# Kernel optimization log

Hardware: AMD Instinct MI355X
Metric: run time of the kernel (lower is better)

Reference implementation:

```python
import jax, jax.numpy as jnp
import numpy as np

B, T_AUX, UP = 4, 75, 110
N_AUX, N_Q, HID, SKIP = 54, 256, 192, 256
K, AUX_K = 6, 3
DIL_FACTS = [0, 1, 2] * 3  # dilation_depth=3, dilation_repeat=3
T = T_AUX * UP - 1  # 8249


def conv1d(x, w, b, dil=1, pad=(0, 0)):
    # x: (B,C,T), w: (O,I,K) torch Conv1d layout
    if pad != (0, 0):
        x = jnp.pad(x, ((0, 0), (0, 0), pad))
    y = jax.lax.conv_general_dilated(x, w, (1,), 'VALID', rhs_dilation=(dil,),
                                     dimension_numbers=('NCH', 'OIH', 'NCH'))
    return y + b[None, :, None]


def setup_inputs() -> dict:
    key = jax.random.key(0)
    ks = jax.random.split(key, 24)
    s = 0.05
    inp = {
        'audio': jax.random.normal(ks[0], (B, N_Q, T), jnp.float32),
        'aux': jax.random.normal(ks[1], (B, N_AUX, T_AUX), jnp.float32),
        'scale_in_w': jax.random.normal(ks[2], (N_AUX, N_AUX, 1), jnp.float32) * s,
        'scale_in_b': jax.random.normal(ks[3], (N_AUX,), jnp.float32) * s,
        'aux0_w': jax.random.normal(ks[4], (N_AUX * 3, N_AUX, AUX_K), jnp.float32) * s,
        'aux0_b': jax.random.normal(ks[5], (N_AUX * 3,), jnp.float32) * s,
        'aux1_w': jax.random.normal(ks[6], (N_AUX * 9, N_AUX * 3, AUX_K), jnp.float32) * s,
        'aux1_b': jax.random.normal(ks[7], (N_AUX * 9,), jnp.float32) * s,
        'up_w': jax.random.normal(ks[8], (UP,), jnp.float32) * s,
        'up_b': jax.random.normal(ks[9], (), jnp.float32) * s,
        'causal_w': jax.random.normal(ks[10], (HID, N_Q, K), jnp.float32) * s,
        'causal_b': jax.random.normal(ks[11], (HID,), jnp.float32) * s,
        'inx_w': jax.random.normal(ks[12], (9, 2 * HID, N_AUX * 9, 1), jnp.float32) * s,
        'inx_b': jax.random.normal(ks[13], (9, 2 * HID), jnp.float32) * s,
        'dilh_w': jax.random.normal(ks[14], (9, 2 * HID, HID, K), jnp.float32) * s,
        'dilh_b': jax.random.normal(ks[15], (9, 2 * HID), jnp.float32) * s,
        'skip_w': jax.random.normal(ks[16], (9, SKIP, HID, 1), jnp.float32) * s,
        'skip_b': jax.random.normal(ks[17], (9, SKIP), jnp.float32) * s,
        'out1_w': jax.random.normal(ks[18], (N_Q, SKIP, 1), jnp.float32) * s,
        'out1_b': jax.random.normal(ks[19], (N_Q,), jnp.float32) * s,
        'out2_w': jax.random.normal(ks[20], (N_Q, N_Q, 1), jnp.float32) * s,
        'out2_b': jax.random.normal(ks[21], (N_Q,), jnp.float32) * s,
    }
    return inp


def reference(audio, aux, scale_in_w, scale_in_b, aux0_w, aux0_b, aux1_w, aux1_b,
              up_w, up_b, causal_w, causal_b, inx_w, inx_b, dilh_w, dilh_b,
              skip_w, skip_b, out1_w, out1_b, out2_w, out2_b):
    # conditioning path: scale_in -> two-sided dilated convs -> deconv upsample
    a = conv1d(aux, scale_in_w, scale_in_b)
    a = conv1d(a, aux0_w, aux0_b, dil=1, pad=(1, 1))      # k=3, dil=1, same length
    a = conv1d(a, aux1_w, aux1_b, dil=3, pad=(3, 3))      # k=3, dil=3, same length
    b_, c_, t_ = a.shape
    x = (a[:, :, :, None] * up_w).reshape(b_, c_, t_ * UP) + up_b  # ConvTranspose2d(1,1,(1,UP))
    x = x[:, :, 1:]  # (B, 486, T)
    # audio path: causal conv (left pad k-1) + softsign
    h = jax.nn.soft_sign(conv1d(audio, causal_w, causal_b, dil=1, pad=(K - 1, 0)))
    sum_out = None
    for l, d in enumerate(DIL_FACTS):
        dil = K ** d
        lpad = dil * (K - 1)  # k**(d+1) - k**d
        xh = conv1d(x, inx_w[l], inx_b[l]) * conv1d(h, dilh_w[l], dilh_b[l], dil=dil, pad=(lpad, 0))
        z = jax.nn.sigmoid(xh[:, :HID])
        h = (1.0 - z) * jnp.tanh(xh[:, HID:]) + z * h
        skip = conv1d(h, skip_w[l], skip_b[l])
        sum_out = skip if sum_out is None else sum_out + skip
    out = conv1d(jax.nn.relu(sum_out), out1_w, out1_b)
    out = conv1d(jax.nn.relu(out), out2_w, out2_b)
    return out.transpose(0, 2, 1)  # (B, T, n_quantize)
```

## Files before the change

kernel.cpp:

```cpp
#include <hip/hip_runtime.h>

#define TLEN 8249
#define TPAD 8320
#define NTILES 130
#define NB 4
#define NAUX 54
#define NQ 256
#define HID 192
#define NSKIP 256
#define KW 6
#define UPF 110
#define TAUX 75
#define PADR 180
#define HROWS (PADR + TPAD)

typedef __attribute__((ext_vector_type(8))) short bf16x8v;
typedef __attribute__((ext_vector_type(4))) float f32x4;

__device__ __forceinline__ unsigned short f2bf(float f) {
  unsigned int u = __float_as_uint(f);
  u += 0x7FFFu + ((u >> 16) & 1u);
  return (unsigned short)(u >> 16);
}

__device__ __forceinline__ f32x4 mfma16(bf16x8v a, bf16x8v b, f32x4 c) {
  return __builtin_amdgcn_mfma_f32_16x16x32_bf16(a, b, c, 0, 0, 0);
}

__global__ void prepack_kernel(
    const float* causal_w, const float* dilh_w, const float* skip_w,
    const float* out1_w, const float* out2_w,
    const float* inx_w, const float* inx_b, const float* up_b,
    unsigned short* pk_causal, unsigned short* pk_dilh, unsigned short* pk_skip,
    unsigned short* pk_out1, unsigned short* pk_out2, float* Cbuf)
{
  int i = blockIdx.x * blockDim.x + threadIdx.x;
  if (i < 9*6*6*24*64*8) {
    int t = i;
    int j = t & 7; t >>= 3;
    int lane = t & 63; t >>= 6;
    int nf = t % 24; t /= 24;
    int kc = t % 6; t /= 6;
    int tap = t % 6; t /= 6;
    int l = t;
    int oc = nf*16 + (lane & 15);
    int ic = kc*32 + ((lane >> 4) << 3) + j;
    pk_dilh[i] = f2bf(dilh_w[((l*384 + oc)*HID + ic)*KW + tap]);
  }
  if (i < 6*8*12*64*8) {
    int t = i;
    int j = t & 7; t >>= 3;
    int lane = t & 63; t >>= 6;
    int nf = t % 12; t /= 12;
    int kc = t % 8; t /= 8;
    int tap = t;
    int oc = nf*16 + (lane & 15);
    int ic = kc*32 + ((lane >> 4) << 3) + j;
    pk_causal[i] = f2bf(causal_w[(oc*NQ + ic)*KW + tap]);
  }
  if (i < 9*6*16*64*8) {
    int t = i;
    int j = t & 7; t >>= 3;
    int lane = t & 63; t >>= 6;
    int nf = t % 16; t /= 16;
    int kc = t % 6; t /= 6;
    int l = t;
    int sc = nf*16 + (lane & 15);
    int ic = kc*32 + ((lane >> 4) << 3) + j;
    pk_skip[i] = f2bf(skip_w[(l*NSKIP + sc)*HID + ic]);
  }
  if (i < 8*16*64*8) {
    int t = i;
    int j = t & 7; t >>= 3;
    int lane = t & 63; t >>= 6;
    int nf = t % 16; t /= 16;
    int kc = t;
    int oq = nf*16 + (lane & 15);
    int sc = kc*32 + ((lane >> 4) << 3) + j;
    pk_out1[i] = f2bf(out1_w[oq*NSKIP + sc]);
    pk_out2[i] = f2bf(out2_w[oq*NQ + sc]);
  }
  if (i < 9*384) {
    int l = i / 384, oc = i % 384;
    const float* wr = inx_w + (l*384 + oc)*486;
    float s = 0.f;
    for (int c = 0; c < 486; c++) s += wr[c];
    Cbuf[i] = up_b[0]*s + inx_b[i];
  }
}

__global__ void zpad_kernel(unsigned short* h_all) {
  int i = blockIdx.x*blockDim.x + threadIdx.x;
  if (i < 9*NB*PADR*HID) {
    int slab = i / (NB*PADR*HID), r = i % (NB*PADR*HID);
    int b = r / (PADR*HID), rr = r % (PADR*HID);
    h_all[((size_t)slab*NB + b)*HROWS*HID + rr] = 0;
  }
}

__global__ void aux1_kernel(const float* aux, const float* w, const float* bias, float* a1) {
  int q = blockIdx.x, b = blockIdx.y, co = threadIdx.x;
  if (co >= NAUX) return;
  float acc = bias[co];
  for (int ci = 0; ci < NAUX; ci++)
    acc += w[co*NAUX + ci] * aux[(b*NAUX + ci)*TAUX + q];
  a1[(b*NAUX + co)*TAUX + q] = acc;
}

__global__ void aux2_kernel(const float* a1, const float* w, const float* bias, float* a2) {
  __shared__ float s[3][NAUX];
  int q = blockIdx.x, b = blockIdx.y, tid = threadIdx.x;
  for (int i = tid; i < 3*NAUX; i += blockDim.x) {
    int k = i / NAUX, c = i % NAUX;
    int qq = q - 1 + k;
    s[k][c] = (qq >= 0 && qq < TAUX) ? a1[(b*NAUX + c)*TAUX + qq] : 0.f;
  }
  __syncthreads();
  int co = tid;
  if (co >= 162) return;
  float acc = bias[co];
  for (int c = 0; c < NAUX; c++)
    #pragma unroll
    for (int k = 0; k < 3; k++)
      acc += w[(co*NAUX + c)*3 + k] * s[k][c];
  a2[(b*162 + co)*TAUX + q] = acc;
}

__global__ void aux3_kernel(const float* a2, const float* w, const float* bias, float* a3) {
  __shared__ float s[3][162];
  int q = blockIdx.x, b = blockIdx.y, tid = threadIdx.x;
  for (int i = tid; i < 3*162; i += blockDim.x) {
    int k = i / 162, c = i % 162;
    int qq = q + 3*(k - 1);
    s[k][c] = (qq >= 0 && qq < TAUX) ? a2[(b*162 + c)*TAUX + qq] : 0.f;
  }
  __syncthreads();
  int co = tid;
  if (co >= 486) return;
  float acc = bias[co];
  for (int c = 0; c < 162; c++)
    #pragma unroll
    for (int k = 0; k < 3; k++)
      acc += w[(co*162 + c)*3 + k] * s[k][c];
  a3[(b*486 + co)*TAUX + q] = acc;
}

__global__ void g_kernel(const float* a3, const float* inx_w, float* G) {
  __shared__ float s[486][15];
  int q0 = blockIdx.x * 15, b = blockIdx.y, l = blockIdx.z;
  int tid = threadIdx.x;
  for (int i = tid; i < 486*15; i += 384) {
    int c = i / 15, qq = i % 15;
    s[c][qq] = a3[(b*486 + c)*TAUX + q0 + qq];
  }
  __syncthreads();
  int oc = tid;
  float acc[15];
  #pragma unroll
  for (int qq = 0; qq < 15; qq++) acc[qq] = 0.f;
  const float* wrow = inx_w + (l*384 + oc)*486;
  for (int c = 0; c < 486; c++) {
    float w = wrow[c];
    #pragma unroll
    for (int qq = 0; qq < 15; qq++) acc[qq] += w * s[c][qq];
  }
  for (int qq = 0; qq < 15; qq++)
    G[((size_t)(l*NB + b)*TAUX + q0 + qq)*384 + oc] = acc[qq];
}

__global__ __launch_bounds__(256, 2)
void causal_kernel(const float* audio, const unsigned short* pk, const float* cb,
                   unsigned short* hbf)
{
  __shared__ __align__(16) unsigned short sA[72*264];
  int b = blockIdx.y, t0 = blockIdx.x*64, tid = threadIdx.x;
  int wv = tid >> 6, lane = tid & 63, lanelo = lane & 15;

  for (int i = tid; i < 72*256; i += 256) {
    int ic = i / 72, tt = i % 72;
    int t = t0 - 5 + tt;
    float v = (t >= 0 && t < TLEN) ? audio[(size_t)(b*NQ + ic)*TLEN + t] : 0.f;
    sA[tt*264 + ic] = f2bf(v);
  }
  __syncthreads();

  f32x4 acc[4][3];
  f32x4 z4 = {0.f, 0.f, 0.f, 0.f};
  #pragma unroll
  for (int m = 0; m < 4; m++)
    #pragma unroll
    for (int i = 0; i < 3; i++) acc[m][i] = z4;

  for (int tap = 0; tap < 6; tap++) {
    for (int kc = 0; kc < 8; kc++) {
      bf16x8v A[4];
      int ko = kc*32 + ((lane >> 4) << 3);
      #pragma unroll
      for (int m = 0; m < 4; m++)
        A[m] = *(const bf16x8v*)&sA[(m*16 + lanelo + tap)*264 + ko];
      #pragma unroll
      for (int i = 0; i < 3; i++) {
        int nf = wv*3 + i;
        bf16x8v Bf = *(const bf16x8v*)&pk[(size_t)((((tap*8) + kc)*12 + nf)*64 + lane)*8];
        #pragma unroll
        for (int m = 0; m < 4; m++) acc[m][i] = mfma16(A[m], Bf, acc[m][i]);
      }
    }
  }

  #pragma unroll
  for (int m = 0; m < 4; m++)
    #pragma unroll
    for (int i = 0; i < 3; i++) {
      int oc = (wv*3 + i)*16 + lanelo;
      float bias = cb[oc];
      #pragma unroll
      for (int r = 0; r < 4; r++) {
        int tl = m*16 + ((lane >> 4) << 2) + r;
        int t = t0 + tl;
        float v = acc[m][i][r] + bias;
        float h0 = v / (1.f + fabsf(v));
        hbf[(size_t)(b*HROWS + t + PADR)*HID + oc] = f2bf(h0);
      }
    }
}

__global__ __launch_bounds__(512, 4)
void layer_kernel(int dil,
                  const unsigned short* __restrict__ hin,
                  unsigned short* __restrict__ hout,
                  const unsigned short* __restrict__ pk_dilh_l,
                  const float* __restrict__ dilh_b_l,
                  const float* __restrict__ Gl, const float* __restrict__ Cl,
                  const float* __restrict__ up_w)
{
  __shared__ __align__(16) unsigned short hs[2][64*192];
  int b = blockIdx.y, t0 = blockIdx.x*64, tid = threadIdx.x;
  int wv = tid >> 6, lane = tid & 63, lanelo = lane & 15, lanehi = lane >> 4;
  int mwv = wv >> 2, nwv = wv & 3;

  const size_t hbase = (size_t)b * HROWS * HID;
  int rowbase0 = t0 - 5*dil + PADR;

  uint4 st[3];
  {
    #pragma unroll
    for (int j = 0; j < 3; j++) {
      int c = tid + j*512, row = c/24, cbk = c%24;
      st[j] = *(const uint4*)&hin[hbase + (size_t)(rowbase0+row)*HID + cbk*8];
    }
    #pragma unroll
    for (int j = 0; j < 3; j++) {
      int c = tid + j*512, row = c/24, cbk = c%24;
      *(uint4*)&hs[0][row*192 + ((cbk ^ (row&7))<<3)] = st[j];
    }
  }

  f32x4 accz[2][3], acct[2][3];
  f32x4 z4 = {0.f, 0.f, 0.f, 0.f};
  #pragma unroll
  for (int m = 0; m < 2; m++)
    #pragma unroll
    for (int i = 0; i < 3; i++) { accz[m][i] = z4; acct[m][i] = z4; }

  for (int tap = 0; tap < 6; tap++) {
    __syncthreads();
    if (tap < 5) {
      int rb = rowbase0 + (tap+1)*dil;
      #pragma unroll
      for (int j = 0; j < 3; j++) {
        int c = tid + j*512, row = c/24, cbk = c%24;
        st[j] = *(const uint4*)&hin[hbase + (size_t)(rb+row)*HID + cbk*8];
      }
    }
    const unsigned short* bufc = hs[tap & 1];
    #pragma unroll
    for (int kc = 0; kc < 6; kc++) {
      bf16x8v A[2];
      #pragma unroll
      for (int m = 0; m < 2; m++) {
        int r = mwv*32 + m*16 + lanelo;
        int cbk = kc*4 + lanehi;
        A[m] = *(const bf16x8v*)&bufc[r*192 + ((cbk ^ (r&7))<<3)];
      }
      #pragma unroll
      for (int i = 0; i < 3; i++) {
        const unsigned short* bp =
            &pk_dilh_l[(size_t)(((tap*6 + kc)*24 + nwv*3 + i)*64 + lane)*8];
        bf16x8v Bz = *(const bf16x8v*)bp;
        bf16x8v Bt = *(const bf16x8v*)(bp + 12*512);
        #pragma unroll
        for (int m = 0; m < 2; m++) {
          accz[m][i] = mfma16(A[m], Bz, accz[m][i]);
          acct[m][i] = mfma16(A[m], Bt, acct[m][i]);
        }
      }
    }
    if (tap < 5) {
      unsigned short* bufn = hs[(tap+1) & 1];
      #pragma unroll
      for (int j = 0; j < 3; j++) {
        int c = tid + j*512, row = c/24, cbk = c%24;
        *(uint4*)&bufn[row*192 + ((cbk ^ (row&7))<<3)] = st[j];
      }
    }
  }

  float izc[3], itc[3], bzc[3], btc[3];
  #pragma unroll
  for (int i = 0; i < 3; i++) {
    int ocz = (nwv*3 + i)*16 + lanelo;
    izc[i] = Cl[ocz];       itc[i] = Cl[192 + ocz];
    bzc[i] = dilh_b_l[ocz]; btc[i] = dilh_b_l[192 + ocz];
  }
  #pragma unroll
  for (int m = 0; m < 2; m++) {
    #pragma unroll
    for (int r = 0; r < 4; r++) {
      int tl = mwv*32 + m*16 + (lanehi << 2) + r;
      int t = t0 + tl;
      int tp1 = t + 1;
      int q = tp1 / UPF; if (q > TAUX - 1) q = TAUX - 1;
      int ui = tp1 - q*UPF; if (ui > UPF - 1) ui = UPF - 1;
      float u = up_w[ui];
      const float* Gb = Gl + (size_t)(b*TAUX + q)*384;
      #pragma unroll
      for (int i = 0; i < 3; i++) {
        int ocz = (nwv*3 + i)*16 + lanelo;
        float iz = u*Gb[ocz]       + izc[i];
        float it = u*Gb[192 + ocz] + itc[i];
        float xz = (accz[m][i][r] + bzc[i]) * iz;
        float xt = (acct[m][i][r] + btc[i]) * it;
        float z  = 1.f / (1.f + __expf(-xz));
        float e2 = __expf(2.f*xt);
        float th = 1.f - 2.f/(e2 + 1.f);
        int cbh = ocz >> 3, jh = ocz & 7;
        unsigned short hob = hs[1][tl*192 + ((cbh ^ (tl&7))<<3) + jh];
        float hold = __uint_as_float(((unsigned int)hob) << 16);
        float hn = (1.f - z)*th + z*hold;
        hout[hbase + (size_t)(t0 + tl + PADR)*HID + ocz] = f2bf(hn);
      }
    }
  }
}

__global__ __launch_bounds__(512, 2)
void skipsum_kernel(const unsigned short* __restrict__ h_all,
                    const unsigned short* __restrict__ pk_skip,
                    const float* __restrict__ skip_b,
                    unsigned short* __restrict__ sbuf)
{
  extern __shared__ __align__(16) unsigned short ss[];
  int b = blockIdx.y, t0 = blockIdx.x*128, tid = threadIdx.x;
  int wv = tid >> 6, lane = tid & 63, lanelo = lane & 15, lanehi = lane >> 4;
  int mwv = wv >> 2, nwv = wv & 3;
  const size_t HS = (size_t)NB * HROWS * HID;

  auto hsrc = [&](int l) {
    int slab = (l == 8) ? 0 : (l + 1);
    return h_all + (size_t)slab*HS + (size_t)b*HROWS*HID + (size_t)(t0 + PADR)*HID;
  };

  uint4 st[6];
  {
    const unsigned short* src = hsrc(0);
    #pragma unroll
    for (int j = 0; j < 6; j++) {
      int c = tid + j*512, row = c/24, cbk = c%24;
      st[j] = *(const uint4*)&src[(size_t)row*HID + cbk*8];
    }
    #pragma unroll
    for (int j = 0; j < 6; j++) {
      int c = tid + j*512, row = c/24, cbk = c%24;
      *(uint4*)&ss[row*192 + ((cbk ^ (row&7))<<3)] = st[j];
    }
  }

  f32x4 acc[4][4];
  f32x4 z4 = {0.f, 0.f, 0.f, 0.f};
  #pragma unroll
  for (int m = 0; m < 4; m++)
    #pragma unroll
    for (int i = 0; i < 4; i++) acc[m][i] = z4;

  for (int l = 0; l < 9; l++) {
    __syncthreads();
    if (l < 8) {
      const unsigned short* src = hsrc(l + 1);
      #pragma unroll
      for (int j = 0; j < 6; j++) {
        int c = tid + j*512, row = c/24, cbk = c%24;
        st[j] = *(const uint4*)&src[(size_t)row*HID + cbk*8];
      }
    }
    const unsigned short* bufc = ss + (l & 1)*(128*192);
    #pragma unroll
    for (int kc = 0; kc < 6; kc++) {
      bf16x8v A[4];
      #pragma unroll
      for (int m = 0; m < 4; m++) {
        int r = mwv*64 + m*16 + lanelo;
        int cbk = kc*4 + lanehi;
        A[m] = *(const bf16x8v*)&bufc[r*192 + ((cbk ^ (r&7))<<3)];
      }
      #pragma unroll
      for (int i = 0; i < 4; i++) {
        bf16x8v Bf = *(const bf16x8v*)
            &pk_skip[(size_t)(((l*6 + kc)*16 + nwv*4 + i)*64 + lane)*8];
        #pragma unroll
        for (int m = 0; m < 4; m++) acc[m][i] = mfma16(A[m], Bf, acc[m][i]);
      }
    }
    if (l < 8) {
      unsigned short* bufn = ss + ((l+1) & 1)*(128*192);
      #pragma unroll
      for (int j = 0; j < 6; j++) {
        int c = tid + j*512, row = c/24, cbk = c%24;
        *(uint4*)&bufn[row*192 + ((cbk ^ (row&7))<<3)] = st[j];
      }
    }
  }

  #pragma unroll
  for (int i = 0; i < 4; i++) {
    int sc = (nwv*4 + i)*16 + lanelo;
    float bias = 0.f;
    #pragma unroll
    for (int l = 0; l < 9; l++) bias += skip_b[l*NSKIP + sc];
    #pragma unroll
    for (int m = 0; m < 4; m++) {
      #pragma unroll
      for (int r = 0; r < 4; r++) {
        int tl = mwv*64 + m*16 + (lanehi << 2) + r;
        float v = acc[m][i][r] + bias;
        sbuf[(size_t)(b*TPAD + t0 + tl)*NSKIP + sc] = f2bf(fmaxf(v, 0.f));
      }
    }
  }
}

__global__ __launch_bounds__(256, 2)
void out_kernel(const unsigned short* sbuf, const unsigned short* pk1, const float* b1,
                const unsigned short* pk2, const float* b2, float* dout)
{
  __shared__ __align__(16) unsigned short s0[64*264];
  int b = blockIdx.y, t0 = blockIdx.x*64, tid = threadIdx.x;
  int wv = tid >> 6, lane = tid & 63, lanelo = lane & 15;
  f32x4 z4 = {0.f, 0.f, 0.f, 0.f};

  for (int i = tid; i < 64*32; i += 256) {
    int r = i >> 5, cbk = i & 31;
    *(uint4*)&s0[r*264 + cbk*8] =
        *(const uint4*)&sbuf[(size_t)(b*TPAD + t0 + r)*NSKIP + cbk*8];
  }
  __syncthreads();

  f32x4 acc[4][4];
  #pragma unroll
  for (int m = 0; m < 4; m++)
    #pragma unroll
    for (int i = 0; i < 4; i++) acc[m][i] = z4;
  for (int kc = 0; kc < 8; kc++) {
    bf16x8v A[4];
    int ko = kc*32 + ((lane >> 4) << 3);
    #pragma unroll
    for (int m = 0; m < 4; m++)
      A[m] = *(const bf16x8v*)&s0[(m*16 + lanelo)*264 + ko];
    #pragma unroll
    for (int i = 0; i < 4; i++) {
      int nf = wv*4 + i;
      bf16x8v Bf = *(const bf16x8v*)&pk1[(size_t)((kc*16 + nf)*64 + lane)*8];
      #pragma unroll
      for (int m = 0; m < 4; m++) acc[m][i] = mfma16(A[m], Bf, acc[m][i]);
    }
  }
  __syncthreads();
  #pragma unroll
  for (int m = 0; m < 4; m++)
    #pragma unroll
    for (int i = 0; i < 4; i++) {
      int oq = (wv*4 + i)*16 + lanelo;
      float bias = b1[oq];
      #pragma unroll
      for (int r = 0; r < 4; r++) {
        int tl = m*16 + ((lane >> 4) << 2) + r;
        float v = acc[m][i][r] + bias;
        s0[tl*264 + oq] = f2bf(fmaxf(v, 0.f));
      }
    }
  __syncthreads();

  #pragma unroll
  for (int m = 0; m < 4; m++)
    #pragma unroll
    for (int i = 0; i < 4; i++) acc[m][i] = z4;
  for (int kc = 0; kc < 8; kc++) {
    bf16x8v A[4];
    int ko = kc*32 + ((lane >> 4) << 3);
    #pragma unroll
    for (int m = 0; m < 4; m++)
      A[m] = *(const bf16x8v*)&s0[(m*16 + lanelo)*264 + ko];
    #pragma unroll
    for (int i = 0; i < 4; i++) {
      int nf = wv*4 + i;
      bf16x8v Bf = *(const bf16x8v*)&pk2[(size_t)((kc*16 + nf)*64 + lane)*8];
      #pragma unroll
      for (int m = 0; m < 4; m++) acc[m][i] = mfma16(A[m], Bf, acc[m][i]);
    }
  }
  #pragma unroll
  for (int m = 0; m < 4; m++)
    #pragma unroll
    for (int i = 0; i < 4; i++) {
      int oq = (wv*4 + i)*16 + lanelo;
      float bias = b2[oq];
      #pragma unroll
      for (int r = 0; r < 4; r++) {
        int tl = m*16 + ((lane >> 4) << 2) + r;
        int t = t0 + tl;
        if (t < TLEN) dout[(size_t)(b*TLEN + t)*NQ + oq] = acc[m][i][r] + bias;
      }
    }
}

extern "C" void kernel_launch(void* const* d_in, const int* in_sizes, int n_in,
                              void* d_out, int out_size, void* d_ws, size_t ws_size,
                              hipStream_t stream)
{
  const float* audio      = (const float*)d_in[0];
  const float* aux        = (const float*)d_in[1];
  const float* scale_in_w = (const float*)d_in[2];
  const float* scale_in_b = (const float*)d_in[3];
  const float* aux0_w     = (const float*)d_in[4];
  const float* aux0_b     = (const float*)d_in[5];
  const float* aux1_w     = (const float*)d_in[6];
  const float* aux1_b     = (const float*)d_in[7];
  const float* up_w       = (const float*)d_in[8];
  const float* up_b       = (const float*)d_in[9];
  const float* causal_w   = (const float*)d_in[10];
  const float* causal_b   = (const float*)d_in[11];
  const float* inx_w      = (const float*)d_in[12];
  const float* inx_b      = (const float*)d_in[13];
  const float* dilh_w     = (const float*)d_in[14];
  const float* dilh_b     = (const float*)d_in[15];
  const float* skip_w     = (const float*)d_in[16];
  const float* skip_b     = (const float*)d_in[17];
  const float* out1_w     = (const float*)d_in[18];
  const float* out1_b     = (const float*)d_in[19];
  const float* out2_w     = (const float*)d_in[20];
  const float* out2_b     = (const float*)d_in[21];

  char* ws = (char*)d_ws;
  size_t off = 0;
  auto alloc = [&](size_t bytes) -> void* {
    void* p = ws + off;
    off += (bytes + 255) & ~(size_t)255;
    return p;
  };
  unsigned short* pk_causal = (unsigned short*)alloc((size_t)6*8*12*64*8*2);
  unsigned short* pk_dilh   = (unsigned short*)alloc((size_t)9*6*6*24*64*8*2);
  unsigned short* pk_skip   = (unsigned short*)alloc((size_t)9*6*16*64*8*2);
  unsigned short* pk_out1   = (unsigned short*)alloc((size_t)8*16*64*8*2);
  unsigned short* pk_out2   = (unsigned short*)alloc((size_t)8*16*64*8*2);
  float* Cbuf    = (float*)alloc((size_t)9*384*4);
  float* a1      = (float*)alloc((size_t)NB*NAUX*TAUX*4);
  float* a2      = (float*)alloc((size_t)NB*162*TAUX*4);
  float* a3      = (float*)alloc((size_t)NB*486*TAUX*4);
  float* Gbuf    = (float*)alloc((size_t)9*NB*TAUX*384*4);
  const size_t HS = (size_t)NB*HROWS*HID;
  unsigned short* h_all = (unsigned short*)alloc((size_t)9*HS*2);
  unsigned short* sbuf  = (unsigned short*)alloc((size_t)NB*TPAD*NSKIP*2);

  hipFuncSetAttribute((const void*)skipsum_kernel,
                      hipFuncAttributeMaxDynamicSharedMemorySize, 2*128*192*2);

  hipLaunchKernelGGL(prepack_kernel, dim3((9*6*6*24*64*8 + 255)/256), dim3(256), 0, stream,
                     causal_w, dilh_w, skip_w, out1_w, out2_w, inx_w, inx_b, up_b,
                     pk_causal, pk_dilh, pk_skip, pk_out1, pk_out2, Cbuf);
  hipLaunchKernelGGL(zpad_kernel, dim3((9*NB*PADR*HID + 255)/256), dim3(256), 0, stream,
                     h_all);
  hipLaunchKernelGGL(aux1_kernel, dim3(TAUX, NB), dim3(64), 0, stream,
                     aux, scale_in_w, scale_in_b, a1);
  hipLaunchKernelGGL(aux2_kernel, dim3(TAUX, NB), dim3(192), 0, stream,
                     a1, aux0_w, aux0_b, a2);
  hipLaunchKernelGGL(aux3_kernel, dim3(TAUX, NB), dim3(512), 0, stream,
                     a2, aux1_w, aux1_b, a3);
  hipLaunchKernelGGL(g_kernel, dim3(5, NB, 9), dim3(384), 0, stream,
                     a3, inx_w, Gbuf);
  hipLaunchKernelGGL(causal_kernel, dim3(NTILES, NB), dim3(256), 0, stream,
                     audio, pk_causal, causal_b, h_all );

  const int dils[9] = {1, 6, 36, 1, 6, 36, 1, 6, 36};
  for (int l = 0; l < 9; l++) {
    const unsigned short* hin = h_all + (size_t)l*HS;
    unsigned short* hout      = (l == 8) ? h_all : h_all + (size_t)(l+1)*HS;
    hipLaunchKernelGGL(layer_kernel, dim3(NTILES, NB), dim3(512), 0, stream,
                       dils[l], hin, hout,
                       pk_dilh + (size_t)l*6*6*24*64*8,
                       dilh_b + (size_t)l*384,
                       Gbuf + (size_t)l*NB*TAUX*384,
                       Cbuf + (size_t)l*384,
                       up_w);
  }

  hipLaunchKernelGGL(skipsum_kernel, dim3(TPAD/128, NB), dim3(512), 2*128*192*2, stream,
                     h_all, pk_skip, skip_b, sbuf);
  hipLaunchKernelGGL(out_kernel, dim3(NTILES, NB), dim3(256), 0, stream,
                     sbuf, pk_out1, out1_b, pk_out2, out2_b, (float*)d_out);
}
```

Before: 1.067 ms.

## Load dilated-conv halo window once into LDS and shrink skipsum tiles

For dilations 1 and 6, the layer kernel loads a single halo window of 64+5*dil rows into shared memory once and reads all six taps from it at shifted row offsets. This replaces six per-tap global reloads that mostly overlapped, and it also supplies the old-h values for the gate from the same buffer. Dilation 36 keeps the double-buffered per-tap path. Separately, skipsum now uses 64-row tiles with static shared memory and targets 4 blocks per CU instead of 2, which gives more blocks and occupancy but less B-fragment reuse per block.

```diff
diff --git a/kernel.cpp b/kernel.cpp
--- a/kernel.cpp
+++ b/kernel.cpp
@@ -242,8 +242,53 @@
   const size_t hbase = (size_t)b * HROWS * HID;
   int rowbase0 = t0 - 5*dil + PADR;
 
-  uint4 st[3];
-  {
+  f32x4 accz[2][3], acct[2][3];
+  f32x4 z4 = {0.f, 0.f, 0.f, 0.f};
+  #pragma unroll
+  for (int m = 0; m < 2; m++)
+    #pragma unroll
+    for (int i = 0; i < 3; i++) { accz[m][i] = z4; acct[m][i] = z4; }
+
+  const unsigned short* holdbuf;
+  int holdoff;
+  unsigned short* flat = &hs[0][0];
+
+  if (dil != 36) {
+    int W = 64 + 5*dil;
+    for (int c = tid; c < W*24; c += 512) {
+      int row = c/24, cbk = c%24;
+      uint4 v = *(const uint4*)&hin[hbase + (size_t)(rowbase0+row)*HID + cbk*8];
+      *(uint4*)&flat[row*192 + ((cbk ^ (row&7))<<3)] = v;
+    }
+    __syncthreads();
+    for (int tap = 0; tap < 6; tap++) {
+      int rb = mwv*32 + lanelo + tap*dil;
+      #pragma unroll
+      for (int kc = 0; kc < 6; kc++) {
+        bf16x8v A[2];
+        #pragma unroll
+        for (int m = 0; m < 2; m++) {
+          int r = rb + m*16;
+          int cbk = kc*4 + lanehi;
+          A[m] = *(const bf16x8v*)&flat[r*192 + ((cbk ^ (r&7))<<3)];
+        }
+        #pragma unroll
+        for (int i = 0; i < 3; i++) {
+          const unsigned short* bp =
+              &pk_dilh_l[(size_t)(((tap*6 + kc)*24 + nwv*3 + i)*64 + lane)*8];
+          bf16x8v Bz = *(const bf16x8v*)bp;
+          bf16x8v Bt = *(const bf16x8v*)(bp + 12*512);
+          #pragma unroll
+          for (int m = 0; m < 2; m++) {
+            accz[m][i] = mfma16(A[m], Bz, accz[m][i]);
+            acct[m][i] = mfma16(A[m], Bt, acct[m][i]);
+          }
+        }
+      }
+    }
+    holdbuf = flat; holdoff = 5*dil;
+  } else {
+    uint4 st[3];
     #pragma unroll
     for (int j = 0; j < 3; j++) {
       int c = tid + j*512, row = c/24, cbk = c%24;
@@ -254,56 +299,49 @@
       int c = tid + j*512, row = c/24, cbk = c%24;
       *(uint4*)&hs[0][row*192 + ((cbk ^ (row&7))<<3)] = st[j];
     }
-  }
-
-  f32x4 accz[2][3], acct[2][3];
-  f32x4 z4 = {0.f, 0.f, 0.f, 0.f};
-  #pragma unroll
-  for (int m = 0; m < 2; m++)
-    #pragma unroll
-    for (int i = 0; i < 3; i++) { accz[m][i] = z4; acct[m][i] = z4; }
-
-  for (int tap = 0; tap < 6; tap++) {
-    __syncthreads();
-    if (tap < 5) {
-      int rb = rowbase0 + (tap+1)*dil;
-      #pragma unroll
-      for (int j = 0; j < 3; j++) {
-        int c = tid + j*512, row = c/24, cbk = c%24;
-        st[j] = *(const uint4*)&hin[hbase + (size_t)(rb+row)*HID + cbk*8];
-      }
-    }
-    const unsigned short* bufc = hs[tap & 1];
-    #pragma unroll
-    for (int kc = 0; kc < 6; kc++) {
-      bf16x8v A[2];
-      #pragma unroll
-      for (int m = 0; m < 2; m++) {
-        int r = mwv*32 + m*16 + lanelo;
-        int cbk = kc*4 + lanehi;
-        A[m] = *(const bf16x8v*)&bufc[r*192 + ((cbk ^ (r&7))<<3)];
-      }
-      #pragma unroll
-      for (int i = 0; i < 3; i++) {
-        const unsigned short* bp =
-            &pk_dilh_l[(size_t)(((tap*6 + kc)*24 + nwv*3 + i)*64 + lane)*8];
-        bf16x8v Bz = *(const bf16x8v*)bp;
-        bf16x8v Bt = *(const bf16x8v*)(bp + 12*512);
+    for (int tap = 0; tap < 6; tap++) {
+      __syncthreads();
+      if (tap < 5) {
+        int rb = rowbase0 + (tap+1)*36;
+        #pragma unroll
+        for (int j = 0; j < 3; j++) {
+          int c = tid + j*512, row = c/24, cbk = c%24;
+          st[j] = *(const uint4*)&hin[hbase + (size_t)(rb+row)*HID + cbk*8];
+        }
+      }
+      const unsigned short* bufc = hs[tap & 1];
+      #pragma unroll
+      for (int kc = 0; kc < 6; kc++) {
+        bf16x8v A[2];
         #pragma unroll
         for (int m = 0; m < 2; m++) {
-          accz[m][i] = mfma16(A[m], Bz, accz[m][i]);
-          acct[m][i] = mfma16(A[m], Bt, acct[m][i]);
+          int r = mwv*32 + m*16 + lanelo;
+          int cbk = kc*4 + lanehi;
+          A[m] = *(const bf16x8v*)&bufc[r*192 + ((cbk ^ (r&7))<<3)];
         }
-      }
-    }
-    if (tap < 5) {
-      unsigned short* bufn = hs[(tap+1) & 1];
-      #pragma unroll
-      for (int j = 0; j < 3; j++) {
-        int c = tid + j*512, row = c/24, cbk = c%24;
-        *(uint4*)&bufn[row*192 + ((cbk ^ (row&7))<<3)] = st[j];
-      }
-    }
+        #pragma unroll
+        for (int i = 0; i < 3; i++) {
+          const unsigned short* bp =
+              &pk_dilh_l[(size_t)(((tap*6 + kc)*24 + nwv*3 + i)*64 + lane)*8];
+          bf16x8v Bz = *(const bf16x8v*)bp;
+          bf16x8v Bt = *(const bf16x8v*)(bp + 12*512);
+          #pragma unroll
+          for (int m = 0; m < 2; m++) {
+            accz[m][i] = mfma16(A[m], Bz, accz[m][i]);
+            acct[m][i] = mfma16(A[m], Bt, acct[m][i]);
+          }
+        }
+      }
+      if (tap < 5) {
+        unsigned short* bufn = hs[(tap+1) & 1];
+        #pragma unroll
+        for (int j = 0; j < 3; j++) {
+          int c = tid + j*512, row = c/24, cbk = c%24;
+          *(uint4*)&bufn[row*192 + ((cbk ^ (row&7))<<3)] = st[j];
+        }
+      }
+    }
+    holdbuf = &hs[1][0]; holdoff = 0;
   }
 
   float izc[3], itc[3], bzc[3], btc[3];
@@ -319,6 +357,7 @@
     for (int r = 0; r < 4; r++) {
       int tl = mwv*32 + m*16 + (lanehi << 2) + r;
       int t = t0 + tl;
+      int hr = tl + holdoff;
       int tp1 = t + 1;
       int q = tp1 / UPF; if (q > TAUX - 1) q = TAUX - 1;
       int ui = tp1 - q*UPF; if (ui > UPF - 1) ui = UPF - 1;
@@ -335,23 +374,23 @@
         float e2 = __expf(2.f*xt);
         float th = 1.f - 2.f/(e2 + 1.f);
         int cbh = ocz >> 3, jh = ocz & 7;
-        unsigned short hob = hs[1][tl*192 + ((cbh ^ (tl&7))<<3) + jh];
+        unsigned short hob = holdbuf[hr*192 + ((cbh ^ (hr&7))<<3) + jh];
         float hold = __uint_as_float(((unsigned int)hob) << 16);
         float hn = (1.f - z)*th + z*hold;
-        hout[hbase + (size_t)(t0 + tl + PADR)*HID + ocz] = f2bf(hn);
-      }
-    }
-  }
-}
-
-__global__ __launch_bounds__(512, 2)
+        hout[hbase + (size_t)(t + PADR)*HID + ocz] = f2bf(hn);
+      }
+    }
+  }
+}
+
+__global__ __launch_bounds__(512, 4)
 void skipsum_kernel(const unsigned short* __restrict__ h_all,
                     const unsigned short* __restrict__ pk_skip,
                     const float* __restrict__ skip_b,
                     unsigned short* __restrict__ sbuf)
 {
-  extern __shared__ __align__(16) unsigned short ss[];
-  int b = blockIdx.y, t0 = blockIdx.x*128, tid = threadIdx.x;
+  __shared__ __align__(16) unsigned short ss[2][64*192];
+  int b = blockIdx.y, t0 = blockIdx.x*64, tid = threadIdx.x;
   int wv = tid >> 6, lane = tid & 63, lanelo = lane & 15, lanehi = lane >> 4;
   int mwv = wv >> 2, nwv = wv & 3;
   const size_t HS = (size_t)NB * HROWS * HID;
@@ -361,25 +400,25 @@
     return h_all + (size_t)slab*HS + (size_t)b*HROWS*HID + (size_t)(t0 + PADR)*HID;
   };
 
-  uint4 st[6];
+  uint4 st[3];
   {
     const unsigned short* src = hsrc(0);
     #pragma unroll
-    for (int j = 0; j < 6; j++) {
+    for (int j = 0; j < 3; j++) {
       int c = tid + j*512, row = c/24, cbk = c%24;
       st[j] = *(const uint4*)&src[(size_t)row*HID + cbk*8];
     }
     #pragma unroll
-    for (int j = 0; j < 6; j++) {
+    for (int j = 0; j < 3; j++) {
       int c = tid + j*512, row = c/24, cbk = c%24;
-      *(uint4*)&ss[row*192 + ((cbk ^ (row&7))<<3)] = st[j];
-    }
-  }
-
-  f32x4 acc[4][4];
+      *(uint4*)&ss[0][row*192 + ((cbk ^ (row&7))<<3)] = st[j];
+    }
+  }
+
+  f32x4 acc[2][4];
   f32x4 z4 = {0.f, 0.f, 0.f, 0.f};
   #pragma unroll
-  for (int m = 0; m < 4; m++)
+  for (int m = 0; m < 2; m++)
     #pragma unroll
     for (int i = 0; i < 4; i++) acc[m][i] = z4;
 
@@ -388,18 +427,18 @@
     if (l < 8) {
       const unsigned short* src = hsrc(l + 1);
       #pragma unroll
-      for (int j = 0; j < 6; j++) {
+      for (int j = 0; j < 3; j++) {
         int c = tid + j*512, row = c/24, cbk = c%24;
         st[j] = *(const uint4*)&src[(size_t)row*HID + cbk*8];
       }
     }
-    const unsigned short* bufc = ss + (l & 1)*(128*192);
+    const unsigned short* bufc = ss[l & 1];
     #pragma unroll
     for (int kc = 0; kc < 6; kc++) {
-      bf16x8v A[4];
-      #pragma unroll
-      for (int m = 0; m < 4; m++) {
-        int r = mwv*64 + m*16 + lanelo;
+      bf16x8v A[2];
+      #pragma unroll
+      for (int m = 0; m < 2; m++) {
+        int r = mwv*32 + m*16 + lanelo;
         int cbk = kc*4 + lanehi;
         A[m] = *(const bf16x8v*)&bufc[r*192 + ((cbk ^ (r&7))<<3)];
       }
@@ -408,13 +447,13 @@
         bf16x8v Bf = *(const bf16x8v*)
             &pk_skip[(size_t)(((l*6 + kc)*16 + nwv*4 + i)*64 + lane)*8];
         #pragma unroll
-        for (int m = 0; m < 4; m++) acc[m][i] = mfma16(A[m], Bf, acc[m][i]);
+        for (int m = 0; m < 2; m++) acc[m][i] = mfma16(A[m], Bf, acc[m][i]);
       }
     }
     if (l < 8) {
-      unsigned short* bufn = ss + ((l+1) & 1)*(128*192);
-      #pragma unroll
-      for (int j = 0; j < 6; j++) {
+      unsigned short* bufn = ss[(l+1) & 1];
+      #pragma unroll
+      for (int j = 0; j < 3; j++) {
         int c = tid + j*512, row = c/24, cbk = c%24;
         *(uint4*)&bufn[row*192 + ((cbk ^ (row&7))<<3)] = st[j];
       }
@@ -428,10 +467,10 @@
     #pragma unroll
     for (int l = 0; l < 9; l++) bias += skip_b[l*NSKIP + sc];
     #pragma unroll
-    for (int m = 0; m < 4; m++) {
+    for (int m = 0; m < 2; m++) {
       #pragma unroll
       for (int r = 0; r < 4; r++) {
-        int tl = mwv*64 + m*16 + (lanehi << 2) + r;
+        int tl = mwv*32 + m*16 + (lanehi << 2) + r;
         float v = acc[m][i][r] + bias;
         sbuf[(size_t)(b*TPAD + t0 + tl)*NSKIP + sc] = f2bf(fmaxf(v, 0.f));
       }
@@ -571,9 +610,6 @@
   unsigned short* h_all = (unsigned short*)alloc((size_t)9*HS*2);
   unsigned short* sbuf  = (unsigned short*)alloc((size_t)NB*TPAD*NSKIP*2);
 
-  hipFuncSetAttribute((const void*)skipsum_kernel,
-                      hipFuncAttributeMaxDynamicSharedMemorySize, 2*128*192*2);
-
   hipLaunchKernelGGL(prepack_kernel, dim3((9*6*6*24*64*8 + 255)/256), dim3(256), 0, stream,
                      causal_w, dilh_w, skip_w, out1_w, out2_w, inx_w, inx_b, up_b,
                      pk_causal, pk_dilh, pk_skip, pk_out1, pk_out2, Cbuf);
@@ -603,7 +639,7 @@
                        up_w);
   }
 
-  hipLaunchKernelGGL(skipsum_kernel, dim3(TPAD/128, NB), dim3(512), 2*128*192*2, stream,
+  hipLaunchKernelGGL(skipsum_kernel, dim3(NTILES, NB), dim3(512), 0, stream,
                      h_all, pk_skip, skip_b, sbuf);
   hipLaunchKernelGGL(out_kernel, dim3(NTILES, NB), dim3(256), 0, stream,
                      sbuf, pk_out1, out1_b, pk_out2, out2_b, (float*)d_out);
```

Measured after the change: 958.5 us. -10.1%, faster.

## Load full dilated halo once per layer tile, fuse skip and output kernels

Applied to the files above, without the earlier changes.

The layer kernel now handles 128 time steps per block. It loads the whole dilated window (128+5*dil rows) into dynamic LDS once, replacing the per-tap double-buffered reloads, so overlapping tap rows are shared. Outputs are staged through LDS for coalesced 16-byte stores in both the causal and layer kernels. The skip-sum and the two output convolutions are fused into one tail kernel, which removes the sbuf round-trip through global memory and writes the final output coalesced via LDS. The cost is much larger LDS use per block (up to about 120KB for dil=36) and half as many blocks, which lowers occupancy and parallelism.

```diff
diff --git a/kernel.cpp b/kernel.cpp
--- a/kernel.cpp
+++ b/kernel.cpp
@@ -3,6 +3,7 @@
 #define TLEN 8249
 #define TPAD 8320
 #define NTILES 130
+#define NTILES2 65
 #define NB 4
 #define NAUX 54
 #define NQ 256
@@ -174,7 +175,7 @@
 {
   __shared__ __align__(16) unsigned short sA[72*264];
   int b = blockIdx.y, t0 = blockIdx.x*64, tid = threadIdx.x;
-  int wv = tid >> 6, lane = tid & 63, lanelo = lane & 15;
+  int wv = tid >> 6, lane = tid & 63, lanelo = lane & 15, lanehi = lane >> 4;
 
   for (int i = tid; i < 72*256; i += 256) {
     int ic = i / 72, tt = i % 72;
@@ -194,7 +195,7 @@
   for (int tap = 0; tap < 6; tap++) {
     for (int kc = 0; kc < 8; kc++) {
       bf16x8v A[4];
-      int ko = kc*32 + ((lane >> 4) << 3);
+      int ko = kc*32 + (lanehi << 3);
       #pragma unroll
       for (int m = 0; m < 4; m++)
         A[m] = *(const bf16x8v*)&sA[(m*16 + lanelo + tap)*264 + ko];
@@ -208,6 +209,7 @@
     }
   }
 
+  unsigned short hv[4][3][4];
   #pragma unroll
   for (int m = 0; m < 4; m++)
     #pragma unroll
@@ -216,16 +218,33 @@
       float bias = cb[oc];
       #pragma unroll
       for (int r = 0; r < 4; r++) {
-        int tl = m*16 + ((lane >> 4) << 2) + r;
-        int t = t0 + tl;
         float v = acc[m][i][r] + bias;
-        float h0 = v / (1.f + fabsf(v));
-        hbf[(size_t)(b*HROWS + t + PADR)*HID + oc] = f2bf(h0);
-      }
-    }
-}
-
-__global__ __launch_bounds__(512, 4)
+        hv[m][i][r] = f2bf(v / (1.f + fabsf(v)));
+      }
+    }
+  __syncthreads();
+  #pragma unroll
+  for (int m = 0; m < 4; m++)
+    #pragma unroll
+    for (int i = 0; i < 3; i++) {
+      int oc = (wv*3 + i)*16 + lanelo;
+      int cbh = oc >> 3, jh = oc & 7;
+      #pragma unroll
+      for (int r = 0; r < 4; r++) {
+        int tl = m*16 + (lanehi << 2) + r;
+        sA[tl*192 + ((cbh ^ (tl&7))<<3) + jh] = hv[m][i][r];
+      }
+    }
+  __syncthreads();
+  #pragma unroll
+  for (int j = 0; j < 6; j++) {
+    int c = tid + j*256, row = c/24, cbk = c%24;
+    uint4 v = *(const uint4*)&sA[row*192 + ((cbk ^ (row&7))<<3)];
+    *(uint4*)&hbf[(size_t)(b*HROWS + t0 + row + PADR)*HID + cbk*8] = v;
+  }
+}
+
+__global__ __launch_bounds__(512, 2)
 void layer_kernel(int dil,
                   const unsigned short* __restrict__ hin,
                   unsigned short* __restrict__ hout,
@@ -234,54 +253,38 @@
                   const float* __restrict__ Gl, const float* __restrict__ Cl,
                   const float* __restrict__ up_w)
 {
-  __shared__ __align__(16) unsigned short hs[2][64*192];
-  int b = blockIdx.y, t0 = blockIdx.x*64, tid = threadIdx.x;
+  extern __shared__ __align__(16) unsigned short flat[];
+  int b = blockIdx.y, t0 = blockIdx.x*128, tid = threadIdx.x;
   int wv = tid >> 6, lane = tid & 63, lanelo = lane & 15, lanehi = lane >> 4;
   int mwv = wv >> 2, nwv = wv & 3;
 
   const size_t hbase = (size_t)b * HROWS * HID;
   int rowbase0 = t0 - 5*dil + PADR;
-
-  uint4 st[3];
-  {
-    #pragma unroll
-    for (int j = 0; j < 3; j++) {
-      int c = tid + j*512, row = c/24, cbk = c%24;
-      st[j] = *(const uint4*)&hin[hbase + (size_t)(rowbase0+row)*HID + cbk*8];
-    }
-    #pragma unroll
-    for (int j = 0; j < 3; j++) {
-      int c = tid + j*512, row = c/24, cbk = c%24;
-      *(uint4*)&hs[0][row*192 + ((cbk ^ (row&7))<<3)] = st[j];
-    }
-  }
-
-  f32x4 accz[2][3], acct[2][3];
+  int W = 128 + 5*dil;
+
+  for (int c = tid; c < W*24; c += 512) {
+    int row = c/24, cbk = c%24;
+    uint4 v = *(const uint4*)&hin[hbase + (size_t)(rowbase0+row)*HID + cbk*8];
+    *(uint4*)&flat[row*192 + ((cbk ^ (row&7))<<3)] = v;
+  }
+  __syncthreads();
+
+  f32x4 accz[4][3], acct[4][3];
   f32x4 z4 = {0.f, 0.f, 0.f, 0.f};
   #pragma unroll
-  for (int m = 0; m < 2; m++)
+  for (int m = 0; m < 4; m++)
     #pragma unroll
     for (int i = 0; i < 3; i++) { accz[m][i] = z4; acct[m][i] = z4; }
 
   for (int tap = 0; tap < 6; tap++) {
-    __syncthreads();
-    if (tap < 5) {
-      int rb = rowbase0 + (tap+1)*dil;
-      #pragma unroll
-      for (int j = 0; j < 3; j++) {
-        int c = tid + j*512, row = c/24, cbk = c%24;
-        st[j] = *(const uint4*)&hin[hbase + (size_t)(rb+row)*HID + cbk*8];
-      }
-    }
-    const unsigned short* bufc = hs[tap & 1];
     #pragma unroll
     for (int kc = 0; kc < 6; kc++) {
-      bf16x8v A[2];
-      #pragma unroll
-      for (int m = 0; m < 2; m++) {
-        int r = mwv*32 + m*16 + lanelo;
+      bf16x8v A[4];
+      #pragma unroll
+      for (int m = 0; m < 4; m++) {
+        int r = mwv*64 + m*16 + lanelo + tap*dil;
         int cbk = kc*4 + lanehi;
-        A[m] = *(const bf16x8v*)&bufc[r*192 + ((cbk ^ (r&7))<<3)];
+        A[m] = *(const bf16x8v*)&flat[r*192 + ((cbk ^ (r&7))<<3)];
       }
       #pragma unroll
       for (int i = 0; i < 3; i++) {
@@ -290,18 +293,10 @@
         bf16x8v Bz = *(const bf16x8v*)bp;
         bf16x8v Bt = *(const bf16x8v*)(bp + 12*512);
         #pragma unroll
-        for (int m = 0; m < 2; m++) {
+        for (int m = 0; m < 4; m++) {
           accz[m][i] = mfma16(A[m], Bz, accz[m][i]);
           acct[m][i] = mfma16(A[m], Bt, acct[m][i]);
         }
-      }
-    }
-    if (tap < 5) {
-      unsigned short* bufn = hs[(tap+1) & 1];
-      #pragma unroll
-      for (int j = 0; j < 3; j++) {
-        int c = tid + j*512, row = c/24, cbk = c%24;
-        *(uint4*)&bufn[row*192 + ((cbk ^ (row&7))<<3)] = st[j];
       }
     }
   }
@@ -313,12 +308,14 @@
     izc[i] = Cl[ocz];       itc[i] = Cl[192 + ocz];
     bzc[i] = dilh_b_l[ocz]; btc[i] = dilh_b_l[192 + ocz];
   }
-  #pragma unroll
-  for (int m = 0; m < 2; m++) {
+  unsigned short hnv[4][4][3];
+  #pragma unroll
+  for (int m = 0; m < 4; m++) {
     #pragma unroll
     for (int r = 0; r < 4; r++) {
-      int tl = mwv*32 + m*16 + (lanehi << 2) + r;
+      int tl = mwv*64 + m*16 + (lanehi << 2) + r;
       int t = t0 + tl;
+      int hr = tl + 5*dil;
       int tp1 = t + 1;
       int q = tp1 / UPF; if (q > TAUX - 1) q = TAUX - 1;
       int ui = tp1 - q*UPF; if (ui > UPF - 1) ui = UPF - 1;
@@ -335,20 +332,42 @@
         float e2 = __expf(2.f*xt);
         float th = 1.f - 2.f/(e2 + 1.f);
         int cbh = ocz >> 3, jh = ocz & 7;
-        unsigned short hob = hs[1][tl*192 + ((cbh ^ (tl&7))<<3) + jh];
+        unsigned short hob = flat[hr*192 + ((cbh ^ (hr&7))<<3) + jh];
         float hold = __uint_as_float(((unsigned int)hob) << 16);
-        float hn = (1.f - z)*th + z*hold;
-        hout[hbase + (size_t)(t0 + tl + PADR)*HID + ocz] = f2bf(hn);
-      }
-    }
+        hnv[m][r][i] = f2bf((1.f - z)*th + z*hold);
+      }
+    }
+  }
+  __syncthreads();
+  #pragma unroll
+  for (int m = 0; m < 4; m++) {
+    #pragma unroll
+    for (int r = 0; r < 4; r++) {
+      int tl = mwv*64 + m*16 + (lanehi << 2) + r;
+      #pragma unroll
+      for (int i = 0; i < 3; i++) {
+        int ocz = (nwv*3 + i)*16 + lanelo;
+        int cbh = ocz >> 3, jh = ocz & 7;
+        flat[tl*192 + ((cbh ^ (tl&7))<<3) + jh] = hnv[m][r][i];
+      }
+    }
+  }
+  __syncthreads();
+  #pragma unroll
+  for (int j = 0; j < 6; j++) {
+    int c = tid + j*512, row = c/24, cbk = c%24;
+    uint4 v = *(const uint4*)&flat[row*192 + ((cbk ^ (row&7))<<3)];
+    *(uint4*)&hout[hbase + (size_t)(t0 + row + PADR)*HID + cbk*8] = v;
   }
 }
 
 __global__ __launch_bounds__(512, 2)
-void skipsum_kernel(const unsigned short* __restrict__ h_all,
-                    const unsigned short* __restrict__ pk_skip,
-                    const float* __restrict__ skip_b,
-                    unsigned short* __restrict__ sbuf)
+void tail_kernel(const unsigned short* __restrict__ h_all,
+                 const unsigned short* __restrict__ pk_skip,
+                 const float* __restrict__ skip_b,
+                 const unsigned short* __restrict__ pk1, const float* __restrict__ b1,
+                 const unsigned short* __restrict__ pk2, const float* __restrict__ b2,
+                 float* __restrict__ dout)
 {
   extern __shared__ __align__(16) unsigned short ss[];
   int b = blockIdx.y, t0 = blockIdx.x*128, tid = threadIdx.x;
@@ -420,6 +439,7 @@
       }
     }
   }
+  __syncthreads();
 
   #pragma unroll
   for (int i = 0; i < 4; i++) {
@@ -433,43 +453,25 @@
       for (int r = 0; r < 4; r++) {
         int tl = mwv*64 + m*16 + (lanehi << 2) + r;
         float v = acc[m][i][r] + bias;
-        sbuf[(size_t)(b*TPAD + t0 + tl)*NSKIP + sc] = f2bf(fmaxf(v, 0.f));
-      }
-    }
-  }
-}
-
-__global__ __launch_bounds__(256, 2)
-void out_kernel(const unsigned short* sbuf, const unsigned short* pk1, const float* b1,
-                const unsigned short* pk2, const float* b2, float* dout)
-{
-  __shared__ __align__(16) unsigned short s0[64*264];
-  int b = blockIdx.y, t0 = blockIdx.x*64, tid = threadIdx.x;
-  int wv = tid >> 6, lane = tid & 63, lanelo = lane & 15;
-  f32x4 z4 = {0.f, 0.f, 0.f, 0.f};
-
-  for (int i = tid; i < 64*32; i += 256) {
-    int r = i >> 5, cbk = i & 31;
-    *(uint4*)&s0[r*264 + cbk*8] =
-        *(const uint4*)&sbuf[(size_t)(b*TPAD + t0 + r)*NSKIP + cbk*8];
-  }
-  __syncthreads();
-
-  f32x4 acc[4][4];
+        ss[tl*264 + sc] = f2bf(fmaxf(v, 0.f));
+      }
+    }
+  }
+  __syncthreads();
+
   #pragma unroll
   for (int m = 0; m < 4; m++)
     #pragma unroll
     for (int i = 0; i < 4; i++) acc[m][i] = z4;
   for (int kc = 0; kc < 8; kc++) {
     bf16x8v A[4];
-    int ko = kc*32 + ((lane >> 4) << 3);
+    int ko = kc*32 + (lanehi << 3);
     #pragma unroll
     for (int m = 0; m < 4; m++)
-      A[m] = *(const bf16x8v*)&s0[(m*16 + lanelo)*264 + ko];
+      A[m] = *(const bf16x8v*)&ss[(mwv*64 + m*16 + lanelo)*264 + ko];
     #pragma unroll
     for (int i = 0; i < 4; i++) {
-      int nf = wv*4 + i;
-      bf16x8v Bf = *(const bf16x8v*)&pk1[(size_t)((kc*16 + nf)*64 + lane)*8];
+      bf16x8v Bf = *(const bf16x8v*)&pk1[(size_t)((kc*16 + nwv*4 + i)*64 + lane)*8];
       #pragma unroll
       for (int m = 0; m < 4; m++) acc[m][i] = mfma16(A[m], Bf, acc[m][i]);
     }
@@ -479,13 +481,13 @@
   for (int m = 0; m < 4; m++)
     #pragma unroll
     for (int i = 0; i < 4; i++) {
-      int oq = (wv*4 + i)*16 + lanelo;
+      int oq = (nwv*4 + i)*16 + lanelo;
       float bias = b1[oq];
       #pragma unroll
       for (int r = 0; r < 4; r++) {
-        int tl = m*16 + ((lane >> 4) << 2) + r;
+        int tl = mwv*64 + m*16 + (lanehi << 2) + r;
         float v = acc[m][i][r] + bias;
-        s0[tl*264 + oq] = f2bf(fmaxf(v, 0.f));
+        ss[tl*264 + oq] = f2bf(fmaxf(v, 0.f));
       }
     }
   __syncthreads();
@@ -496,31 +498,47 @@
     for (int i = 0; i < 4; i++) acc[m][i] = z4;
   for (int kc = 0; kc < 8; kc++) {
     bf16x8v A[4];
-    int ko = kc*32 + ((lane >> 4) << 3);
+    int ko = kc*32 + (lanehi << 3);
     #pragma unroll
     for (int m = 0; m < 4; m++)
-      A[m] = *(const bf16x8v*)&s0[(m*16 + lanelo)*264 + ko];
+      A[m] = *(const bf16x8v*)&ss[(mwv*64 + m*16 + lanelo)*264 + ko];
     #pragma unroll
     for (int i = 0; i < 4; i++) {
-      int nf = wv*4 + i;
-      bf16x8v Bf = *(const bf16x8v*)&pk2[(size_t)((kc*16 + nf)*64 + lane)*8];
+      bf16x8v Bf = *(const bf16x8v*)&pk2[(size_t)((kc*16 + nwv*4 + i)*64 + lane)*8];
       #pragma unroll
       for (int m = 0; m < 4; m++) acc[m][i] = mfma16(A[m], Bf, acc[m][i]);
     }
   }
-  #pragma unroll
-  for (int m = 0; m < 4; m++)
-    #pragma unroll
-    for (int i = 0; i < 4; i++) {
-      int oq = (wv*4 + i)*16 + lanelo;
-      float bias = b2[oq];
-      #pragma unroll
-      for (int r = 0; r < 4; r++) {
-        int tl = m*16 + ((lane >> 4) << 2) + r;
-        int t = t0 + tl;
-        if (t < TLEN) dout[(size_t)(b*TLEN + t)*NQ + oq] = acc[m][i][r] + bias;
-      }
-    }
+  float* so2 = (float*)ss;
+  #pragma unroll
+  for (int p = 0; p < 2; p++) {
+    __syncthreads();
+    if (mwv == p) {
+      #pragma unroll
+      for (int m = 0; m < 4; m++) {
+        #pragma unroll
+        for (int i = 0; i < 4; i++) {
+          int oq = (nwv*4 + i)*16 + lanelo;
+          float bias = b2[oq];
+          #pragma unroll
+          for (int r = 0; r < 4; r++) {
+            int lr = m*16 + (lanehi << 2) + r;
+            so2[lr*260 + oq] = acc[m][i][r] + bias;
+          }
+        }
+      }
+    }
+    __syncthreads();
+    #pragma unroll
+    for (int j = 0; j < 8; j++) {
+      int c = tid + j*512, row = c >> 6, ch = c & 63;
+      int t = t0 + p*64 + row;
+      if (t < TLEN) {
+        uint4 v = *(const uint4*)&so2[row*260 + ch*4];
+        *(uint4*)&dout[(size_t)(b*TLEN + t)*NQ + ch*4] = v;
+      }
+    }
+  }
 }
 
 extern "C" void kernel_launch(void* const* d_in, const int* in_sizes, int n_in,
@@ -569,10 +587,11 @@
   float* Gbuf    = (float*)alloc((size_t)9*NB*TAUX*384*4);
   const size_t HS = (size_t)NB*HROWS*HID;
   unsigned short* h_all = (unsigned short*)alloc((size_t)9*HS*2);
-  unsigned short* sbuf  = (unsigned short*)alloc((size_t)NB*TPAD*NSKIP*2);
-
-  hipFuncSetAttribute((const void*)skipsum_kernel,
-                      hipFuncAttributeMaxDynamicSharedMemorySize, 2*128*192*2);
+
+  hipFuncSetAttribute((const void*)layer_kernel,
+                      hipFuncAttributeMaxDynamicSharedMemorySize, 120000);
+  hipFuncSetAttribute((const void*)tail_kernel,
+                      hipFuncAttributeMaxDynamicSharedMemorySize, 98304);
 
   hipLaunchKernelGGL(prepack_kernel, dim3((9*6*6*24*64*8 + 255)/256), dim3(256), 0, stream,
                      causal_w, dilh_w, skip_w, out1_w, out2_w, inx_w, inx_b, up_b,
@@ -594,7 +613,8 @@
   for (int l = 0; l < 9; l++) {
     const unsigned short* hin = h_all + (size_t)l*HS;
     unsigned short* hout      = (l == 8) ? h_all : h_all + (size_t)(l+1)*HS;
-    hipLaunchKernelGGL(layer_kernel, dim3(NTILES, NB), dim3(512), 0, stream,
+    int ldsb = (128 + 5*dils[l]) * 192 * 2;
+    hipLaunchKernelGGL(layer_kernel, dim3(NTILES2, NB), dim3(512), ldsb, stream,
                        dils[l], hin, hout,
                        pk_dilh + (size_t)l*6*6*24*64*8,
                        dilh_b + (size_t)l*384,
@@ -603,8 +623,7 @@
                        up_w);
   }
 
-  hipLaunchKernelGGL(skipsum_kernel, dim3(TPAD/128, NB), dim3(512), 2*128*192*2, stream,
-                     h_all, pk_skip, skip_b, sbuf);
-  hipLaunchKernelGGL(out_kernel, dim3(NTILES, NB), dim3(256), 0, stream,
-                     sbuf, pk_out1, out1_b, pk_out2, out2_b, (float*)d_out);
-}
+  hipLaunchKernelGGL(tail_kernel, dim3(NTILES2, NB), dim3(512), 98304, stream,
+                     h_all, pk_skip, skip_b, pk_out1, out1_b, pk_out2, out2_b,
+                     (float*)d_out);
+}
```

New measurement: 991.7 us. 7.0% less time.
